# Kernel optimization log

Measured on AMD Instinct MI355X. Metric: run time of the kernel, lower is better.

The kernel has to match this reference:

```python
import jax, jax.numpy as jnp
from jax import lax
import numpy as np

B, T, H, K = 128, 256, 768, 64


def setup_inputs() -> dict:
    key = jax.random.key(0)
    k1, k2, k3, k4 = jax.random.split(key, 4)
    hidden = jax.random.normal(k1, (B, T, H), dtype=jnp.float32)
    masks = jnp.ones((B, T), dtype=jnp.int32)
    target = jax.random.randint(k2, (B, T), 0, K, dtype=jnp.int32)
    W = jax.random.normal(k3, (H, K), dtype=jnp.float32) * 0.02
    b = jnp.zeros((K,), dtype=jnp.float32)
    transitions = jax.random.uniform(k4, (K, K), dtype=jnp.float32)
    return {"hidden": hidden, "masks": masks, "target": target,
            "W": W, "b": b, "transitions": transitions}


def _crf_log_norm(emissions, trans, seq_len):
    # emissions: [B,T,K]; forward algorithm (log-sum-exp recurrence over time)
    Tn = emissions.shape[1]
    alpha0 = emissions[:, 0]  # [B,K]

    def step(alpha, xs):
        emis_t, t = xs
        new = jax.nn.logsumexp(alpha[:, :, None] + trans[None], axis=1) + emis_t
        alpha = jnp.where((t < seq_len)[:, None], new, alpha)
        return alpha, None

    xs = (jnp.swapaxes(emissions[:, 1:], 0, 1), jnp.arange(1, Tn))
    alpha, _ = lax.scan(step, alpha0, xs)
    return jax.nn.logsumexp(alpha, axis=1)  # [B]


def _crf_sequence_score(emissions, tags, trans, seq_len):
    Tn = emissions.shape[1]
    t_idx = jnp.arange(Tn)
    valid = t_idx[None, :] < seq_len[:, None]  # [B,T]
    unary = jnp.take_along_axis(emissions, tags[..., None], axis=2)[..., 0]
    unary = jnp.sum(jnp.where(valid, unary, 0.0), axis=1)
    pair = trans[tags[:, :-1], tags[:, 1:]]  # [B,T-1]
    valid_pair = t_idx[1:][None, :] < seq_len[:, None]
    binary = jnp.sum(jnp.where(valid_pair, pair, 0.0), axis=1)
    return unary + binary


def _crf_decode(emissions, trans, seq_len):
    # Viterbi with backpointers; padded steps carry state (identity backptr)
    Bn, Tn, Kn = emissions.shape
    v0 = emissions[:, 0]

    def step(v, xs):
        emis_t, t = xs
        scores = v[:, :, None] + trans[None]  # [B, K_prev, K_cur]
        bp = jnp.argmax(scores, axis=1).astype(jnp.int32)
        new_v = jnp.max(scores, axis=1) + emis_t
        m = (t < seq_len)[:, None]
        v = jnp.where(m, new_v, v)
        bp = jnp.where(m, bp, jnp.arange(Kn, dtype=jnp.int32)[None])
        return v, bp

    xs = (jnp.swapaxes(emissions[:, 1:], 0, 1), jnp.arange(1, Tn))
    v, bps = lax.scan(step, v0, xs)  # bps: [T-1, B, K]
    best_score = jnp.max(v, axis=1)
    last_tag = jnp.argmax(v, axis=1).astype(jnp.int32)

    def back(tag, bp_t):
        prev = jnp.take_along_axis(bp_t, tag[:, None], axis=1)[:, 0]
        return prev, prev

    _, rev_tags = lax.scan(back, last_tag, bps, reverse=True)  # [T-1, B]
    path = jnp.concatenate([rev_tags, last_tag[None]], axis=0)  # [T, B]
    path = jnp.swapaxes(path, 0, 1)  # [B, T]
    valid = jnp.arange(Tn)[None, :] < seq_len[:, None]
    path = jnp.where(valid, path, 0)
    return path, best_score


def reference(hidden, masks, target, W, b, transitions):
    # dense projection (dropout omitted for determinism)
    emissions = jnp.einsum('bth,hk->btk', hidden, W) + b  # [B,T,K]
    seq_len = jnp.sum(masks, axis=1).astype(jnp.int32)
    log_norm = _crf_log_norm(emissions, transitions, seq_len)
    seq_score = _crf_sequence_score(emissions, target, transitions, seq_len)
    log_likelihood = seq_score - log_norm  # [B]
    decode_predict, _crf_scores = _crf_decode(emissions, transitions, seq_len)
    return decode_predict, log_likelihood
```

## Files before the change

kernel.cpp:

```cpp
#include <hip/hip_runtime.h>

#define B_ 128
#define T_ 256
#define H_ 768
#define K_ 64
#define BT_ (B_ * T_)

template <int CTRL>
__device__ __forceinline__ float dpp_mov_f(float x) {
    return __int_as_float(__builtin_amdgcn_update_dpp(
        __float_as_int(x), __float_as_int(x), CTRL, 0xF, 0xF, false));
}
__device__ __forceinline__ float wave_max64(float x) {
    x = fmaxf(x, dpp_mov_f<0x111>(x));
    x = fmaxf(x, dpp_mov_f<0x112>(x));
    x = fmaxf(x, dpp_mov_f<0x114>(x));
    x = fmaxf(x, dpp_mov_f<0x118>(x));
    x = fmaxf(x, dpp_mov_f<0x142>(x));
    x = fmaxf(x, dpp_mov_f<0x143>(x));
    return __int_as_float(__builtin_amdgcn_readlane(__float_as_int(x), 63));
}
__device__ __forceinline__ float readlane0_f(float x) {
    return __int_as_float(__builtin_amdgcn_readfirstlane(__float_as_int(x)));
}
template <int I>
__device__ __forceinline__ float readlane_f(float x) {
    return __int_as_float(__builtin_amdgcn_readlane(__float_as_int(x), I));
}

#define BK_ 32
#define P_ 130
__global__ __launch_bounds__(256) void gemm_emis(const float* __restrict__ hidden,
                                                 const float* __restrict__ W,
                                                 const float* __restrict__ bias,
                                                 float* __restrict__ emis) {
    __shared__ float At[BK_ * P_];

    const int tid = threadIdx.x;
    const int lane = tid & 63;
    const int wc = __builtin_amdgcn_readfirstlane((tid >> 6) * 16);
    const int rowbase = blockIdx.x * 128;
    const int srow = tid >> 3;
    const int sh4 = tid & 7;

    float acc0[16], acc1[16];
#pragma unroll
    for (int c = 0; c < 16; ++c) { acc0[c] = bias[wc + c]; acc1[c] = acc0[c]; }

    float4 pf[4];
#pragma unroll
    for (int i = 0; i < 4; ++i)
        pf[i] = *(const float4*)&hidden[(rowbase + srow + i * 32) * H_ + sh4 * 4];

    for (int kb = 0; kb < H_ / BK_; ++kb) {
        __syncthreads();
#pragma unroll
        for (int i = 0; i < 4; ++i) {
            int row = srow + i * 32;
            At[(sh4 * 4 + 0) * P_ + row] = pf[i].x;
            At[(sh4 * 4 + 1) * P_ + row] = pf[i].y;
            At[(sh4 * 4 + 2) * P_ + row] = pf[i].z;
            At[(sh4 * 4 + 3) * P_ + row] = pf[i].w;
        }
        __syncthreads();
        if (kb + 1 < H_ / BK_) {
#pragma unroll
            for (int i = 0; i < 4; ++i)
                pf[i] = *(const float4*)&hidden[(rowbase + srow + i * 32) * H_ +
                                                (kb + 1) * BK_ + sh4 * 4];
        }
        const float* Wk = &W[(kb * BK_) * K_ + wc];
#pragma unroll 8
        for (int h = 0; h < BK_; ++h) {
            float2 a = *(const float2*)&At[h * P_ + 2 * lane];
            float4 w0 = *(const float4*)&Wk[h * K_ + 0];
            float4 w1 = *(const float4*)&Wk[h * K_ + 4];
            float4 w2 = *(const float4*)&Wk[h * K_ + 8];
            float4 w3 = *(const float4*)&Wk[h * K_ + 12];
            acc0[0]  += a.x * w0.x; acc1[0]  += a.y * w0.x;
            acc0[1]  += a.x * w0.y; acc1[1]  += a.y * w0.y;
            acc0[2]  += a.x * w0.z; acc1[2]  += a.y * w0.z;
            acc0[3]  += a.x * w0.w; acc1[3]  += a.y * w0.w;
            acc0[4]  += a.x * w1.x; acc1[4]  += a.y * w1.x;
            acc0[5]  += a.x * w1.y; acc1[5]  += a.y * w1.y;
            acc0[6]  += a.x * w1.z; acc1[6]  += a.y * w1.z;
            acc0[7]  += a.x * w1.w; acc1[7]  += a.y * w1.w;
            acc0[8]  += a.x * w2.x; acc1[8]  += a.y * w2.x;
            acc0[9]  += a.x * w2.y; acc1[9]  += a.y * w2.y;
            acc0[10] += a.x * w2.z; acc1[10] += a.y * w2.z;
            acc0[11] += a.x * w2.w; acc1[11] += a.y * w2.w;
            acc0[12] += a.x * w3.x; acc1[12] += a.y * w3.x;
            acc0[13] += a.x * w3.y; acc1[13] += a.y * w3.y;
            acc0[14] += a.x * w3.z; acc1[14] += a.y * w3.z;
            acc0[15] += a.x * w3.w; acc1[15] += a.y * w3.w;
        }
    }

    float* e0 = &emis[(size_t)(rowbase + 2 * lane) * K_ + wc];
    float* e1 = &emis[(size_t)(rowbase + 2 * lane + 1) * K_ + wc];
#pragma unroll
    for (int q = 0; q < 4; ++q) {
        *(float4*)&e0[q * 4] = make_float4(acc0[q * 4], acc0[q * 4 + 1],
                                           acc0[q * 4 + 2], acc0[q * 4 + 3]);
        *(float4*)&e1[q * 4] = make_float4(acc1[q * 4], acc1[q * 4 + 1],
                                           acc1[q * 4 + 2], acc1[q * 4 + 3]);
    }
}

__global__ __launch_bounds__(128, 1) void crf_kernel(const float* __restrict__ emis,
                                                     const int* __restrict__ masks,
                                                     const int* __restrict__ target,
                                                     const float* __restrict__ trans,
                                                     float* __restrict__ out) {
    __shared__ __align__(16) float ebuf[T_ * K_];
    __shared__ __align__(16) float vbuf[T_ * K_];
    __shared__ float tbuf[K_ * 65];

    const int tid = threadIdx.x;
    const int lane = tid & 63;
    const int b = blockIdx.x;
    const float* eb = emis + (size_t)b * (T_ * K_);

    {
        const float4* src = (const float4*)eb;
        float4* dst = (float4*)ebuf;
#pragma unroll
        for (int k = 0; k < 32; ++k) dst[tid + k * 128] = src[tid + k * 128];
    }
    int sl = 0;
#pragma unroll
    for (int k = 0; k < 4; ++k) sl += masks[b * T_ + lane + k * 64];
#pragma unroll
    for (int m = 32; m; m >>= 1) sl += __shfl_xor(sl, m, 64);
    const int seq_len = sl;
    __syncthreads();

    if (tid < 64) {
        float Ecol[64];
#pragma unroll
        for (int i = 0; i < 64; ++i) Ecol[i] = __expf(trans[i * K_ + lane]);

        float e_c = ebuf[lane];
        float e00 = readlane0_f(e_c);
        float p = __expf(e_c - e00);
        float C = e00;
        float logD0prev = 0.f;
        float e_n = ebuf[K_ + lane];
        float en0 = readlane0_f(e_n);
        float xg = __expf(e_n - en0);

        for (int t = 1; t < T_; ++t) {
            float e_f = (t < T_ - 1) ? ebuf[(t + 1) * K_ + lane] : 0.f;
            float a0 = 0.f, a1 = 0.f, a2 = 0.f, a3 = 0.f;
            float a4 = 0.f, a5 = 0.f, a6 = 0.f, a7 = 0.f;
#define FWD8(base)                                                     \
            a0 = fmaf(readlane_f<base + 0>(p), Ecol[base + 0], a0);    \
            a1 = fmaf(readlane_f<base + 1>(p), Ecol[base + 1], a1);    \
            a2 = fmaf(readlane_f<base + 2>(p), Ecol[base + 2], a2);    \
            a3 = fmaf(readlane_f<base + 3>(p), Ecol[base + 3], a3);    \
            a4 = fmaf(readlane_f<base + 4>(p), Ecol[base + 4], a4);    \
            a5 = fmaf(readlane_f<base + 5>(p), Ecol[base + 5], a5);    \
            a6 = fmaf(readlane_f<base + 6>(p), Ecol[base + 6], a6);    \
            a7 = fmaf(readlane_f<base + 7>(p), Ecol[base + 7], a7);
            FWD8(0) FWD8(8) FWD8(16) FWD8(24) FWD8(32) FWD8(40) FWD8(48) FWD8(56)
#undef FWD8
            float D = ((a0 + a1) + (a2 + a3)) + ((a4 + a5) + (a6 + a7));
            float pnew = D * xg;
            if (t < seq_len) { p = pnew; C += en0 + logD0prev; }
            float D0 = readlane0_f(D);
            logD0prev = __logf(D0);
            float gn = __fdividef(1.f, D0);
            en0 = readlane0_f(e_f);
            xg = __expf(e_f - en0) * gn;
            e_n = e_f;
        }
        float rs = p;
#pragma unroll
        for (int m = 32; m; m >>= 1) rs += __shfl_xor(rs, m, 64);
        float log_norm = C + __logf(rs);

        float sc = 0.f;
#pragma unroll
        for (int k = 0; k < 4; ++k) {
            int t = lane + k * 64;
            if (t < seq_len) {
                int tg = target[b * T_ + t];
                sc += ebuf[t * K_ + tg];
                if (t >= 1) sc += trans[target[b * T_ + t - 1] * K_ + tg];
            }
        }
#pragma unroll
        for (int m = 32; m; m >>= 1) sc += __shfl_xor(sc, m, 64);
        if (lane == 0) out[BT_ + b] = sc - log_norm;
    } else {
        float Tcol[64];
#pragma unroll
        for (int i = 0; i < 64; ++i) Tcol[i] = trans[i * K_ + lane];
        for (int idx = lane; idx < K_ * K_; idx += 64)
            tbuf[(idx >> 6) * 65 + (idx & 63)] = trans[idx];

        float v = ebuf[lane];
        vbuf[lane] = v;
        float e_n = ebuf[K_ + lane];
        for (int t = 1; t < T_; ++t) {
            float e_f = (t < T_ - 1) ? ebuf[(t + 1) * K_ + lane] : 0.f;
            float m0 = -3.4e38f, m1 = m0, m2 = m0, m3 = m0;
            float m4 = m0, m5 = m0, m6 = m0, m7 = m0;
#define VIT8(base)                                                        \
            m0 = fmaxf(m0, readlane_f<base + 0>(v) + Tcol[base + 0]);     \
            m1 = fmaxf(m1, readlane_f<base + 1>(v) + Tcol[base + 1]);     \
            m2 = fmaxf(m2, readlane_f<base + 2>(v) + Tcol[base + 2]);     \
            m3 = fmaxf(m3, readlane_f<base + 3>(v) + Tcol[base + 3]);     \
            m4 = fmaxf(m4, readlane_f<base + 4>(v) + Tcol[base + 4]);     \
            m5 = fmaxf(m5, readlane_f<base + 5>(v) + Tcol[base + 5]);     \
            m6 = fmaxf(m6, readlane_f<base + 6>(v) + Tcol[base + 6]);     \
            m7 = fmaxf(m7, readlane_f<base + 7>(v) + Tcol[base + 7]);
            VIT8(0) VIT8(8) VIT8(16) VIT8(24) VIT8(32) VIT8(40) VIT8(48) VIT8(56)
#undef VIT8
            float M = fmaxf(fmaxf(fmaxf(m0, m1), fmaxf(m2, m3)),
                            fmaxf(fmaxf(m4, m5), fmaxf(m6, m7)));
            float vn = M + e_n;
            if (t < seq_len) v = vn;
            vbuf[t * K_ + lane] = v;
            e_n = e_f;
        }

        float M = wave_max64(v);
        unsigned long long ball = __ballot(v >= M);
        int tag = (int)__builtin_ctzll(ball);

        int path[4];
#pragma unroll
        for (int k = 0; k < 4; ++k) path[k] = 0;
        if (lane == ((T_ - 1) & 63)) path[(T_ - 1) >> 6] = tag;

        float vpre = vbuf[(T_ - 2) * K_ + lane];
        for (int t = T_ - 1; t >= 1; --t) {
            float vnext = (t >= 2) ? vbuf[(t - 2) * K_ + lane] : 0.f;
            if (t < seq_len) {
                float s = vpre + tbuf[lane * 65 + tag];
                float Ms = wave_max64(s);
                unsigned long long bl = __ballot(s >= Ms);
                tag = (int)__builtin_ctzll(bl);
            }
            int pidx = t - 1;
            if (lane == (pidx & 63)) path[pidx >> 6] = tag;
            vpre = vnext;
        }
#pragma unroll
        for (int k = 0; k < 4; ++k) {
            int t = lane + k * 64;
            out[b * T_ + t] = (t < seq_len) ? (float)path[k] : 0.f;
        }
    }
}

extern "C" void kernel_launch(void* const* d_in, const int* in_sizes, int n_in,
                              void* d_out, int out_size, void* d_ws, size_t ws_size,
                              hipStream_t stream) {
    const float* hidden = (const float*)d_in[0];
    const int* masks    = (const int*)d_in[1];
    const int* target   = (const int*)d_in[2];
    const float* W      = (const float*)d_in[3];
    const float* bias   = (const float*)d_in[4];
    const float* trans  = (const float*)d_in[5];
    float* out = (float*)d_out;
    float* emis = (float*)d_ws;

    gemm_emis<<<dim3(BT_ / 128), dim3(256), 0, stream>>>(hidden, W, bias, emis);
    crf_kernel<<<dim3(B_), dim3(128), 0, stream>>>(emis, masks, target, trans, out);
}
```

Before: 377.9 us.

## Split CRF forward and Viterbi into separate blocks; shrink GEMM tile

The CRF kernel now launches 2*B single-wave blocks, so the forward log-normaliser and the Viterbi decode for each sequence run in separate blocks instead of two waves of one block. Emissions are read directly from global memory, with no staging copy into LDS. The emission GEMM tile drops from 128 to 64 rows per block, with launch bounds asking for 2 blocks per CU, to get more blocks and occupancy. The cost is serial global loads sitting inside the recurrence loops, and each sequence's emissions being read twice.

```diff
diff --git a/kernel.cpp b/kernel.cpp
--- a/kernel.cpp
+++ b/kernel.cpp
@@ -28,131 +28,110 @@
     return __int_as_float(__builtin_amdgcn_readlane(__float_as_int(x), I));
 }
 
-#define BK_ 32
-#define P_ 130
-__global__ __launch_bounds__(256) void gemm_emis(const float* __restrict__ hidden,
-                                                 const float* __restrict__ W,
-                                                 const float* __restrict__ bias,
-                                                 float* __restrict__ emis) {
-    __shared__ float At[BK_ * P_];
+#define GBK 32
+#define GP 66
+__global__ __launch_bounds__(256, 2) void gemm_emis(const float* __restrict__ hidden,
+                                                    const float* __restrict__ W,
+                                                    const float* __restrict__ bias,
+                                                    float* __restrict__ emis) {
+    __shared__ float At[GBK * GP];
 
     const int tid = threadIdx.x;
     const int lane = tid & 63;
-    const int wc = __builtin_amdgcn_readfirstlane((tid >> 6) * 16);
-    const int rowbase = blockIdx.x * 128;
+    const int wv = tid >> 6;
+    const int rp = lane & 31;
+    const int ch = lane >> 5;
+    const int colbase = wv * 16 + ch * 8;
+    const int rowbase = blockIdx.x * 64;
     const int srow = tid >> 3;
     const int sh4 = tid & 7;
 
-    float acc0[16], acc1[16];
-#pragma unroll
-    for (int c = 0; c < 16; ++c) { acc0[c] = bias[wc + c]; acc1[c] = acc0[c]; }
-
-    float4 pf[4];
-#pragma unroll
-    for (int i = 0; i < 4; ++i)
-        pf[i] = *(const float4*)&hidden[(rowbase + srow + i * 32) * H_ + sh4 * 4];
-
-    for (int kb = 0; kb < H_ / BK_; ++kb) {
+    float acc0[8], acc1[8];
+#pragma unroll
+    for (int c = 0; c < 8; ++c) { acc0[c] = bias[colbase + c]; acc1[c] = acc0[c]; }
+
+    float4 pf[2];
+#pragma unroll
+    for (int i = 0; i < 2; ++i)
+        pf[i] = *(const float4*)&hidden[(size_t)(rowbase + srow + i * 32) * H_ + sh4 * 4];
+
+    for (int kb = 0; kb < H_ / GBK; ++kb) {
         __syncthreads();
 #pragma unroll
-        for (int i = 0; i < 4; ++i) {
+        for (int i = 0; i < 2; ++i) {
             int row = srow + i * 32;
-            At[(sh4 * 4 + 0) * P_ + row] = pf[i].x;
-            At[(sh4 * 4 + 1) * P_ + row] = pf[i].y;
-            At[(sh4 * 4 + 2) * P_ + row] = pf[i].z;
-            At[(sh4 * 4 + 3) * P_ + row] = pf[i].w;
+            At[(sh4 * 4 + 0) * GP + row] = pf[i].x;
+            At[(sh4 * 4 + 1) * GP + row] = pf[i].y;
+            At[(sh4 * 4 + 2) * GP + row] = pf[i].z;
+            At[(sh4 * 4 + 3) * GP + row] = pf[i].w;
         }
         __syncthreads();
-        if (kb + 1 < H_ / BK_) {
-#pragma unroll
-            for (int i = 0; i < 4; ++i)
-                pf[i] = *(const float4*)&hidden[(rowbase + srow + i * 32) * H_ +
-                                                (kb + 1) * BK_ + sh4 * 4];
-        }
-        const float* Wk = &W[(kb * BK_) * K_ + wc];
-#pragma unroll 8
-        for (int h = 0; h < BK_; ++h) {
-            float2 a = *(const float2*)&At[h * P_ + 2 * lane];
+        if (kb + 1 < H_ / GBK) {
+#pragma unroll
+            for (int i = 0; i < 2; ++i)
+                pf[i] = *(const float4*)&hidden[(size_t)(rowbase + srow + i * 32) * H_ +
+                                                (kb + 1) * GBK + sh4 * 4];
+        }
+        const float* Wk = &W[(size_t)(kb * GBK) * K_ + colbase];
+#pragma unroll 4
+        for (int h = 0; h < GBK; ++h) {
+            float2 a = *(const float2*)&At[h * GP + 2 * rp];
             float4 w0 = *(const float4*)&Wk[h * K_ + 0];
             float4 w1 = *(const float4*)&Wk[h * K_ + 4];
-            float4 w2 = *(const float4*)&Wk[h * K_ + 8];
-            float4 w3 = *(const float4*)&Wk[h * K_ + 12];
-            acc0[0]  += a.x * w0.x; acc1[0]  += a.y * w0.x;
-            acc0[1]  += a.x * w0.y; acc1[1]  += a.y * w0.y;
-            acc0[2]  += a.x * w0.z; acc1[2]  += a.y * w0.z;
-            acc0[3]  += a.x * w0.w; acc1[3]  += a.y * w0.w;
-            acc0[4]  += a.x * w1.x; acc1[4]  += a.y * w1.x;
-            acc0[5]  += a.x * w1.y; acc1[5]  += a.y * w1.y;
-            acc0[6]  += a.x * w1.z; acc1[6]  += a.y * w1.z;
-            acc0[7]  += a.x * w1.w; acc1[7]  += a.y * w1.w;
-            acc0[8]  += a.x * w2.x; acc1[8]  += a.y * w2.x;
-            acc0[9]  += a.x * w2.y; acc1[9]  += a.y * w2.y;
-            acc0[10] += a.x * w2.z; acc1[10] += a.y * w2.z;
-            acc0[11] += a.x * w2.w; acc1[11] += a.y * w2.w;
-            acc0[12] += a.x * w3.x; acc1[12] += a.y * w3.x;
-            acc0[13] += a.x * w3.y; acc1[13] += a.y * w3.y;
-            acc0[14] += a.x * w3.z; acc1[14] += a.y * w3.z;
-            acc0[15] += a.x * w3.w; acc1[15] += a.y * w3.w;
+            acc0[0] += a.x * w0.x; acc1[0] += a.y * w0.x;
+            acc0[1] += a.x * w0.y; acc1[1] += a.y * w0.y;
+            acc0[2] += a.x * w0.z; acc1[2] += a.y * w0.z;
+            acc0[3] += a.x * w0.w; acc1[3] += a.y * w0.w;
+            acc0[4] += a.x * w1.x; acc1[4] += a.y * w1.x;
+            acc0[5] += a.x * w1.y; acc1[5] += a.y * w1.y;
+            acc0[6] += a.x * w1.z; acc1[6] += a.y * w1.z;
+            acc0[7] += a.x * w1.w; acc1[7] += a.y * w1.w;
         }
     }
 
-    float* e0 = &emis[(size_t)(rowbase + 2 * lane) * K_ + wc];
-    float* e1 = &emis[(size_t)(rowbase + 2 * lane + 1) * K_ + wc];
-#pragma unroll
-    for (int q = 0; q < 4; ++q) {
-        *(float4*)&e0[q * 4] = make_float4(acc0[q * 4], acc0[q * 4 + 1],
-                                           acc0[q * 4 + 2], acc0[q * 4 + 3]);
-        *(float4*)&e1[q * 4] = make_float4(acc1[q * 4], acc1[q * 4 + 1],
-                                           acc1[q * 4 + 2], acc1[q * 4 + 3]);
-    }
-}
-
-__global__ __launch_bounds__(128, 1) void crf_kernel(const float* __restrict__ emis,
-                                                     const int* __restrict__ masks,
-                                                     const int* __restrict__ target,
-                                                     const float* __restrict__ trans,
-                                                     float* __restrict__ out) {
-    __shared__ __align__(16) float ebuf[T_ * K_];
+    float* e0 = &emis[(size_t)(rowbase + 2 * rp) * K_ + colbase];
+    float* e1 = &emis[(size_t)(rowbase + 2 * rp + 1) * K_ + colbase];
+    *(float4*)&e0[0] = make_float4(acc0[0], acc0[1], acc0[2], acc0[3]);
+    *(float4*)&e0[4] = make_float4(acc0[4], acc0[5], acc0[6], acc0[7]);
+    *(float4*)&e1[0] = make_float4(acc1[0], acc1[1], acc1[2], acc1[3]);
+    *(float4*)&e1[4] = make_float4(acc1[4], acc1[5], acc1[6], acc1[7]);
+}
+
+__global__ __launch_bounds__(64, 1) void crf_kernel(const float* __restrict__ emis,
+                                                    const int* __restrict__ masks,
+                                                    const int* __restrict__ target,
+                                                    const float* __restrict__ trans,
+                                                    float* __restrict__ out) {
     __shared__ __align__(16) float vbuf[T_ * K_];
     __shared__ float tbuf[K_ * 65];
 
-    const int tid = threadIdx.x;
-    const int lane = tid & 63;
-    const int b = blockIdx.x;
-    const float* eb = emis + (size_t)b * (T_ * K_);
-
-    {
-        const float4* src = (const float4*)eb;
-        float4* dst = (float4*)ebuf;
-#pragma unroll
-        for (int k = 0; k < 32; ++k) dst[tid + k * 128] = src[tid + k * 128];
-    }
+    const int lane = threadIdx.x;
+    const int bid = blockIdx.x;
+    const int b = bid & (B_ - 1);
+
     int sl = 0;
 #pragma unroll
     for (int k = 0; k < 4; ++k) sl += masks[b * T_ + lane + k * 64];
 #pragma unroll
     for (int m = 32; m; m >>= 1) sl += __shfl_xor(sl, m, 64);
     const int seq_len = sl;
-    __syncthreads();
-
-    if (tid < 64) {
+
+    const float* eb = emis + (size_t)b * (T_ * K_);
+
+    if (bid < B_) {
         float Ecol[64];
 #pragma unroll
         for (int i = 0; i < 64; ++i) Ecol[i] = __expf(trans[i * K_ + lane]);
 
-        float e_c = ebuf[lane];
+        float e_c = eb[lane];
         float e00 = readlane0_f(e_c);
         float p = __expf(e_c - e00);
         float C = e00;
         float logD0prev = 0.f;
-        float e_n = ebuf[K_ + lane];
+        float e_n = eb[K_ + lane];
         float en0 = readlane0_f(e_n);
         float xg = __expf(e_n - en0);
 
-        for (int t = 1; t < T_; ++t) {
-            float e_f = (t < T_ - 1) ? ebuf[(t + 1) * K_ + lane] : 0.f;
-            float a0 = 0.f, a1 = 0.f, a2 = 0.f, a3 = 0.f;
-            float a4 = 0.f, a5 = 0.f, a6 = 0.f, a7 = 0.f;
 #define FWD8(base)                                                     \
             a0 = fmaf(readlane_f<base + 0>(p), Ecol[base + 0], a0);    \
             a1 = fmaf(readlane_f<base + 1>(p), Ecol[base + 1], a1);    \
@@ -162,8 +141,12 @@
             a5 = fmaf(readlane_f<base + 5>(p), Ecol[base + 5], a5);    \
             a6 = fmaf(readlane_f<base + 6>(p), Ecol[base + 6], a6);    \
             a7 = fmaf(readlane_f<base + 7>(p), Ecol[base + 7], a7);
+
+        for (int t = 1; t < T_; ++t) {
+            float e_f = (t < T_ - 1) ? eb[(t + 1) * K_ + lane] : 0.f;
+            float a0 = 0.f, a1 = 0.f, a2 = 0.f, a3 = 0.f;
+            float a4 = 0.f, a5 = 0.f, a6 = 0.f, a7 = 0.f;
             FWD8(0) FWD8(8) FWD8(16) FWD8(24) FWD8(32) FWD8(40) FWD8(48) FWD8(56)
-#undef FWD8
             float D = ((a0 + a1) + (a2 + a3)) + ((a4 + a5) + (a6 + a7));
             float pnew = D * xg;
             if (t < seq_len) { p = pnew; C += en0 + logD0prev; }
@@ -174,6 +157,7 @@
             xg = __expf(e_f - en0) * gn;
             e_n = e_f;
         }
+#undef FWD8
         float rs = p;
 #pragma unroll
         for (int m = 32; m; m >>= 1) rs += __shfl_xor(rs, m, 64);
@@ -185,7 +169,7 @@
             int t = lane + k * 64;
             if (t < seq_len) {
                 int tg = target[b * T_ + t];
-                sc += ebuf[t * K_ + tg];
+                sc += eb[t * K_ + tg];
                 if (t >= 1) sc += trans[target[b * T_ + t - 1] * K_ + tg];
             }
         }
@@ -199,13 +183,10 @@
         for (int idx = lane; idx < K_ * K_; idx += 64)
             tbuf[(idx >> 6) * 65 + (idx & 63)] = trans[idx];
 
-        float v = ebuf[lane];
+        float v = eb[lane];
         vbuf[lane] = v;
-        float e_n = ebuf[K_ + lane];
-        for (int t = 1; t < T_; ++t) {
-            float e_f = (t < T_ - 1) ? ebuf[(t + 1) * K_ + lane] : 0.f;
-            float m0 = -3.4e38f, m1 = m0, m2 = m0, m3 = m0;
-            float m4 = m0, m5 = m0, m6 = m0, m7 = m0;
+        float e_n = eb[K_ + lane];
+
 #define VIT8(base)                                                        \
             m0 = fmaxf(m0, readlane_f<base + 0>(v) + Tcol[base + 0]);     \
             m1 = fmaxf(m1, readlane_f<base + 1>(v) + Tcol[base + 1]);     \
@@ -215,8 +196,12 @@
             m5 = fmaxf(m5, readlane_f<base + 5>(v) + Tcol[base + 5]);     \
             m6 = fmaxf(m6, readlane_f<base + 6>(v) + Tcol[base + 6]);     \
             m7 = fmaxf(m7, readlane_f<base + 7>(v) + Tcol[base + 7]);
+
+        for (int t = 1; t < T_; ++t) {
+            float e_f = (t < T_ - 1) ? eb[(t + 1) * K_ + lane] : 0.f;
+            float m0 = -3.4e38f, m1 = m0, m2 = m0, m3 = m0;
+            float m4 = m0, m5 = m0, m6 = m0, m7 = m0;
             VIT8(0) VIT8(8) VIT8(16) VIT8(24) VIT8(32) VIT8(40) VIT8(48) VIT8(56)
-#undef VIT8
             float M = fmaxf(fmaxf(fmaxf(m0, m1), fmaxf(m2, m3)),
                             fmaxf(fmaxf(m4, m5), fmaxf(m6, m7)));
             float vn = M + e_n;
@@ -224,6 +209,7 @@
             vbuf[t * K_ + lane] = v;
             e_n = e_f;
         }
+#undef VIT8
 
         float M = wave_max64(v);
         unsigned long long ball = __ballot(v >= M);
@@ -267,6 +253,6 @@
     float* out = (float*)d_out;
     float* emis = (float*)d_ws;
 
-    gemm_emis<<<dim3(BT_ / 128), dim3(256), 0, stream>>>(hidden, W, bias, emis);
-    crf_kernel<<<dim3(B_), dim3(128), 0, stream>>>(emis, masks, target, trans, out);
-}
+    gemm_emis<<<dim3(BT_ / 64), dim3(256), 0, stream>>>(hidden, W, bias, emis);
+    crf_kernel<<<dim3(2 * B_), dim3(64), 0, stream>>>(emis, masks, target, trans, out);
+}
```

Result: no change. 381.5 us (+0.9%).
